# Optimization experiments

Hardware: AMD Instinct MI355X
Metric: run time of the kernel (lower is better)

The kernel has to match this reference:

```python
import jax, jax.numpy as jnp
import numpy as np

N = 50000        # num_node
P = 256          # nfeat
M = 128          # nhid
E = 800000       # num edges
KAPPA = 0.9
MITR = 20        # fixed-point iterations (orig: up to 300 w/ tol; fixed count for jit)
POWER_ITERS = 100


def proj_norm_inf(W, v):
    """Project each row of W onto the L1 ball of radius v (torch projection_norm_inf)."""
    m = W.shape[-1]
    a = jnp.abs(W)
    u = jnp.sort(a, axis=-1)[:, ::-1]                       # sorted desc
    cssv = jnp.cumsum(u, axis=-1) - v
    ind = jnp.arange(1, m + 1, dtype=W.dtype)
    rho = jnp.maximum(jnp.sum(u * ind > cssv, axis=-1), 1)
    theta = jnp.take_along_axis(cssv, (rho - 1)[:, None], axis=-1)[:, 0] / rho.astype(W.dtype)
    proj = jnp.sign(W) * jnp.maximum(a - theta[:, None], 0.0)
    return jnp.where((a.sum(-1) > v)[:, None], proj, W)


def spmm_AT(rows, cols, vals, Y):
    """A^T @ Y for COO A: out[c] = sum_e vals[e] * Y[rows[e]] where cols[e]==c. Y: [n, d]."""
    return jax.ops.segment_sum(vals[:, None] * Y[rows], cols, num_segments=N)


def spectral_rad(rows, cols, vals):
    """Power iteration for spectral radius of sparse A (torch get_spectral_rad)."""
    v0 = jnp.ones((N,), vals.dtype) / np.sqrt(N)

    def body(i, carry):
        v, _ = carry
        w = jax.ops.segment_sum(vals * v[cols], rows, num_segments=N)  # A @ v
        r = jnp.linalg.norm(w)
        return (w / (r + 1e-12), r)

    _, rho = jax.lax.fori_loop(0, POWER_ITERS, body, (v0, jnp.float32(1.0)))
    return jax.lax.stop_gradient(rho)


def implicit_graph(W, Omega, U, rows, cols, vals, adj_rho):
    """One ImplicitGraph layer: fixed point X = relu(W X A + Omega U A), X: [m, n]."""
    Wp = proj_norm_inf(W, KAPPA / adj_rho)
    # b_Omega = Omega @ U @ A, computed as (A^T @ (U^T @ Omega^T))^T : [m, n]
    B = spmm_AT(rows, cols, vals, U.T @ Omega.T).T

    def step(X, _):
        Xn = jax.nn.relu(spmm_AT(rows, cols, vals, (Wp @ X).T).T + B)
        return Xn, None

    X, _ = jax.lax.scan(jax.checkpoint(step), B, None, length=MITR)  # X_0 = b_Omega
    return X


def setup_inputs():
    key = jax.random.key(0)
    ks = jax.random.split(key, 10)
    s = lambda d: 1.0 / np.sqrt(d)
    return {
        "features": jax.random.normal(ks[0], (P, N), jnp.float32),
        "edge_vals": jax.random.uniform(ks[1], (E,), jnp.float32) * 0.1,
        "W1": jax.random.normal(ks[2], (M, M), jnp.float32) * s(M),
        "Omega1": jax.random.normal(ks[3], (M, P), jnp.float32) * s(P),
        "W2": jax.random.normal(ks[4], (M, M), jnp.float32) * s(M),
        "Omega2": jax.random.normal(ks[5], (M, M), jnp.float32) * s(M),
        "V0_w": jax.random.normal(ks[6], (M, P), jnp.float32) * s(P),
        "V0_b": jnp.zeros((M,), jnp.float32),
        "V1_w": jax.random.normal(ks[7], (M, M), jnp.float32) * s(M),
        "V1_b": jnp.zeros((M,), jnp.float32),
        "edge_rows": jax.random.randint(ks[8], (E,), 0, N),
        "edge_cols": jax.random.randint(ks[9], (E,), 0, N),
    }


def reference(features, edge_vals, W1, Omega1, W2, Omega2, V0_w, V0_b, V1_w, V1_b,
              edge_rows, edge_cols):
    adj_rho = spectral_rad(edge_rows, edge_cols, edge_vals)
    x = features                                                           # [p, n]
    h = implicit_graph(W1, Omega1, x, edge_rows, edge_cols, edge_vals, adj_rho)  # [m, n]
    x = jax.nn.elu(h.T + x.T @ V0_w.T + V0_b).T                            # [m, n]
    h = implicit_graph(W2, Omega2, x, edge_rows, edge_cols, edge_vals, adj_rho)
    out = h.T + x.T @ V1_w.T + V1_b                                        # [n, m]
    return out  # F.dropout is identity in eval mode
```

## Files before the change

### kernel.cpp

```cpp
#include <hip/hip_runtime.h>
#include <hip/hip_fp16.h>
#include <math.h>

#define NNODE 50000
#define NEDGE 800000
#define PITR  12
#define MITR  20
#define NBLK  196
#define NPAD  50048
#define ECAP  512

typedef _Float16 half8 __attribute__((ext_vector_type(8)));
typedef float floatx4 __attribute__((ext_vector_type(4)));


__global__ __launch_bounds__(256) void init_kernel(int* __restrict__ cnt_col,
                                                   float* __restrict__ wA,
                                                   float* __restrict__ norms) {
    int i = blockIdx.x * 256 + threadIdx.x;
    if (i < NNODE) { cnt_col[i] = 0; wA[i] = 1.0f; }
    if (i <= PITR) norms[i] = (i == 0) ? (float)NNODE : 0.0f;
}

__global__ __launch_bounds__(256) void count_kernel(const int* __restrict__ cols,
                                                    int* __restrict__ cnt_col) {
    int e = blockIdx.x * 256 + threadIdx.x;
    if (e < NEDGE) atomicAdd(&cnt_col[cols[e]], 1);
}

__global__ __launch_bounds__(256) void block_sums(const int* __restrict__ cnt,
                                                  int* __restrict__ bsum) {
    int i = blockIdx.x * 256 + threadIdx.x;
    int x = (i < NNODE) ? cnt[i] : 0;
    __shared__ int s[256];
    s[threadIdx.x] = x; __syncthreads();
    for (int off = 128; off; off >>= 1) {
        if (threadIdx.x < off) s[threadIdx.x] += s[threadIdx.x + off];
        __syncthreads();
    }
    if (threadIdx.x == 0) bsum[blockIdx.x] = s[0];
}

__global__ __launch_bounds__(256) void scan_partials(const int* __restrict__ bsum,
                                                     int* __restrict__ boff,
                                                     int* __restrict__ col_start) {
    __shared__ int s[256];
    int tid = threadIdx.x;
    int x = (tid < NBLK) ? bsum[tid] : 0;
    s[tid] = x; __syncthreads();
    for (int off = 1; off < 256; off <<= 1) {
        int t = (tid >= off) ? s[tid - off] : 0;
        __syncthreads();
        s[tid] += t;
        __syncthreads();
    }
    if (tid < NBLK) boff[tid] = s[tid] - x;
    if (tid == 255) col_start[NNODE] = s[255];
}

__global__ __launch_bounds__(256) void scan_final(const int* __restrict__ cnt,
                                                  const int* __restrict__ boff,
                                                  int* __restrict__ col_start,
                                                  int* __restrict__ cur) {
    int b = blockIdx.x, tid = threadIdx.x;
    int i = b * 256 + tid;
    int x = (i < NNODE) ? cnt[i] : 0;
    __shared__ int s[256];
    s[tid] = x; __syncthreads();
    for (int off = 1; off < 256; off <<= 1) {
        int t = (tid >= off) ? s[tid - off] : 0;
        __syncthreads();
        s[tid] += t;
        __syncthreads();
    }
    if (i < NNODE) { int excl = boff[b] + s[tid] - x; col_start[i] = excl; cur[i] = excl; }
}

__global__ __launch_bounds__(256) void fill_kernel(const int* __restrict__ rows,
                                                   const int* __restrict__ cols,
                                                   const float* __restrict__ vals,
                                                   int* __restrict__ cur_col,
                                                   int2* __restrict__ csc) {
    int e = blockIdx.x * 256 + threadIdx.x;
    if (e >= NEDGE) return;
    int c = cols[e];
    int pc = atomicAdd(&cur_col[c], 1);
    csc[pc] = make_int2(rows[e], __float_as_int(vals[e]));
}

__global__ __launch_bounds__(256) void spmv_pow(const int* __restrict__ col_start,
                                                const int2* __restrict__ csc,
                                                const float* __restrict__ wprev,
                                                float* __restrict__ wnew,
                                                const float* __restrict__ norm_in,
                                                float* __restrict__ norm_out) {
    int gid = blockIdx.x * 256 + threadIdx.x;
    int c = gid >> 2, sub = gid & 3;
    float inv = 1.0f / (sqrtf(*norm_in) + 1e-12f);
    float acc = 0.0f;
    if (c < NNODE) {
        int e0 = col_start[c], e1 = col_start[c + 1];
        for (int e = e0 + sub; e < e1; e += 4) {
            int2 ev = csc[e];
            acc += __int_as_float(ev.y) * wprev[ev.x];
        }
    }
    acc += __shfl_xor(acc, 1, 64);
    acc += __shfl_xor(acc, 2, 64);
    acc *= inv;
    float sq = (sub == 0 && c < NNODE) ? acc * acc : 0.0f;
    if (sub == 0 && c < NNODE) wnew[c] = acc;
    #pragma unroll
    for (int o = 32; o > 0; o >>= 1) sq += __shfl_down(sq, o, 64);
    __shared__ float wsum[4];
    int lane = threadIdx.x & 63, wv = threadIdx.x >> 6;
    if (lane == 0) wsum[wv] = sq;
    __syncthreads();
    if (threadIdx.x == 0) atomicAdd(norm_out, wsum[0] + wsum[1] + wsum[2] + wsum[3]);
}

__global__ __launch_bounds__(128) void proj_kernel(const float* __restrict__ Wa, const float* __restrict__ Wb,
                                                   __half* __restrict__ Oa, __half* __restrict__ Ob,
                                                   const float* __restrict__ norms) {
    __shared__ float u[128];
    __shared__ float sc[128];
    __shared__ float cs[128];
    __shared__ int ci[128];
    float rho = sqrtf(norms[PITR]);
    float vcap = 0.9f / rho;
    int which = blockIdx.x >> 7, row = blockIdx.x & 127;
    const float* W = which ? Wb : Wa;
    __half* O = which ? Ob : Oa;
    int j = threadIdx.x;
    float wv = W[row * 128 + j];
    float a = fabsf(wv);
    sc[j] = a; __syncthreads();
    for (int off = 64; off > 0; off >>= 1) {
        if (j < off) sc[j] += sc[j + off];
        __syncthreads();
    }
    float asum = sc[0];
    __syncthreads();
    if (asum <= vcap) { O[row * 128 + j] = (__half)wv; return; }
    u[j] = a; __syncthreads();
    for (int k = 2; k <= 128; k <<= 1) {
        for (int st = k >> 1; st > 0; st >>= 1) {
            int l = j ^ st;
            if (l > j) {
                float mine = u[j], other = u[l];
                bool sw = ((j & k) == 0) ? (mine < other) : (mine > other);
                if (sw) { u[j] = other; u[l] = mine; }
            }
            __syncthreads();
        }
    }
    sc[j] = u[j]; __syncthreads();
    for (int off = 1; off < 128; off <<= 1) {
        float t = (j >= off) ? sc[j - off] : 0.f;
        __syncthreads();
        sc[j] += t;
        __syncthreads();
    }
    float cssv = sc[j] - vcap;
    cs[j] = cssv;
    ci[j] = (u[j] * (float)(j + 1) > cssv) ? 1 : 0;
    __syncthreads();
    for (int off = 64; off > 0; off >>= 1) {
        if (j < off) ci[j] += ci[j + off];
        __syncthreads();
    }
    int cnt = ci[0]; if (cnt < 1) cnt = 1;
    float theta = cs[cnt - 1] / (float)cnt;
    float pr = fmaxf(a - theta, 0.f);
    O[row * 128 + j] = (__half)((wv < 0.f) ? -pr : pr);
}

__global__ __launch_bounds__(256) void wf_pack(const __half* __restrict__ Wp1, __half* __restrict__ Wf1,
                                               const __half* __restrict__ Wp2, __half* __restrict__ Wf2) {
    int which = blockIdx.x >> 3;
    int t = (blockIdx.x & 7) * 256 + threadIdx.x;
    const __half* Wp = which ? Wp2 : Wp1;
    __half* Wf = which ? Wf2 : Wf1;
    int lane = t & 63, frag = t >> 6;
    int ks = frag >> 3, it = frag & 7;
    int row = it * 16 + (lane & 15);
    int col = ks * 32 + (lane >> 4) * 8;
    *(uint4*)(Wf + (size_t)t * 8) = *(const uint4*)(Wp + (size_t)row * 128 + col);
}

template<int K>
__global__ __launch_bounds__(256) void wfpack32(const float* __restrict__ W, __half* __restrict__ Wf) {
    int t = blockIdx.x * 256 + threadIdx.x;
    int lane = t & 63, frag = t >> 6;
    int ks = frag >> 3, it = frag & 7;
    int row = it * 16 + (lane & 15);
    int col = ks * 32 + (lane >> 4) * 8;
    float4 a = *(const float4*)(W + (size_t)row * K + col);
    float4 b = *(const float4*)(W + (size_t)row * K + col + 4);
    union { uint4 u; __half2 h[4]; } pk;
    pk.h[0] = __float22half2_rn(make_float2(a.x, a.y));
    pk.h[1] = __float22half2_rn(make_float2(a.z, a.w));
    pk.h[2] = __float22half2_rn(make_float2(b.x, b.y));
    pk.h[3] = __float22half2_rn(make_float2(b.z, b.w));
    *(uint4*)(Wf + (size_t)t * 8) = pk.u;
}

__global__ __launch_bounds__(256) void feat_t(const float* __restrict__ F, __half* __restrict__ Fh, int n) {
    __shared__ unsigned short T[64 * 264];
    int nd0 = blockIdx.x * 64;
    int tid = threadIdx.x;
    for (int kk = 0; kk < 64; kk++) {
        int k = kk * 4 + (tid >> 6);
        int node = tid & 63;
        float v = (nd0 + node < n) ? F[(size_t)k * n + nd0 + node] : 0.f;
        __half h = (__half)v;
        T[node * 264 + k] = *(unsigned short*)&h;
    }
    __syncthreads();
    #pragma unroll
    for (int j = 0; j < 8; j++) {
        int row = j * 8 + (tid >> 5);
        int k8 = (tid & 31) * 8;
        uint4 v = *(const uint4*)&T[row * 264 + k8];
        if (nd0 + row < n) *(uint4*)(Fh + (size_t)(nd0 + row) * 256 + k8) = v;
    }
}

template<int K, int ACT, bool HASADD, bool HASBIAS, bool OUTF32>
__global__ __launch_bounds__(256) void gemmx(const _Float16* __restrict__ Wf,
                                             const _Float16* __restrict__ Xsrc,
                                             const __half* __restrict__ ADDh,
                                             const float* __restrict__ bias,
                                             void* __restrict__ Cout,
                                             int n) {
    __shared__ unsigned short Xs[128 * 136];
    int tid = threadIdx.x, wv = tid >> 6, lane = tid & 63;
    int node0 = blockIdx.x * 128;
    floatx4 acc[2][8];
    #pragma unroll
    for (int m = 0; m < 2; m++)
        #pragma unroll
        for (int it = 0; it < 8; it++) acc[m][it] = (floatx4)0.f;

    for (int kc = 0; kc < K; kc += 128) {
        if (kc) __syncthreads();
        #pragma unroll
        for (int j = 0; j < 8; j++) {
            int row = j * 16 + (tid >> 4), col = (tid & 15) * 8;
            uint4 v = *(const uint4*)(Xsrc + (size_t)(node0 + row) * K + kc + col);
            *(uint4*)&Xs[row * 136 + col] = v;
        }
        __syncthreads();
        int xrow = wv * 32 + (lane & 15), koff = (lane >> 4) * 8;
        #pragma unroll
        for (int ks = 0; ks < 4; ks++) {
            int k0 = ks * 32 + koff;
            half8 x0 = *(const half8*)&Xs[xrow * 136 + k0];
            half8 x1 = *(const half8*)&Xs[(xrow + 16) * 136 + k0];
            int ksg = (kc >> 5) + ks;
            #pragma unroll
            for (int it = 0; it < 8; it++) {
                half8 w = *(const half8*)(Wf + ((size_t)(ksg * 8 + it) * 64 + lane) * 8);
                acc[0][it] = __builtin_amdgcn_mfma_f32_16x16x32_f16(w, x0, acc[0][it], 0, 0, 0);
                acc[1][it] = __builtin_amdgcn_mfma_f32_16x16x32_f16(w, x1, acc[1][it], 0, 0, 0);
            }
        }
    }

    int i0 = (lane >> 4) * 4;
    #pragma unroll
    for (int m = 0; m < 2; m++) {
        int nl = wv * 32 + m * 16 + (lane & 15);
        int nd = node0 + nl;
        #pragma unroll
        for (int it = 0; it < 8; it++) {
            float o[4];
            #pragma unroll
            for (int r = 0; r < 4; r++) o[r] = acc[m][it][r];
            if (HASADD) {
                if (nd < n) {
                    union { uint2 u; __half2 h[2]; } av;
                    av.u = *(const uint2*)(ADDh + (size_t)nd * 128 + it * 16 + i0);
                    float2 a0 = __half22float2(av.h[0]), a1 = __half22float2(av.h[1]);
                    o[0] += a0.x; o[1] += a0.y; o[2] += a1.x; o[3] += a1.y;
                }
            }
            if (HASBIAS) {
                float4 bv = *(const float4*)(bias + it * 16 + i0);
                o[0] += bv.x; o[1] += bv.y; o[2] += bv.z; o[3] += bv.w;
            }
            if (ACT == 1) {
                #pragma unroll
                for (int r = 0; r < 4; r++) o[r] = fmaxf(o[r], 0.f);
            } else if (ACT == 2) {
                #pragma unroll
                for (int r = 0; r < 4; r++) o[r] = (o[r] > 0.f) ? o[r] : expm1f(o[r]);
            }
            union { uint2 u; __half2 h[2]; } pk;
            pk.h[0] = __float22half2_rn(make_float2(o[0], o[1]));
            pk.h[1] = __float22half2_rn(make_float2(o[2], o[3]));
            *(uint2*)&Xs[nl * 136 + it * 16 + i0] = pk.u;
        }
    }
    if (OUTF32) {
        float* C = (float*)Cout;
        #pragma unroll
        for (int j = 0; j < 16; j++) {
            int rl = wv * 32 + j * 2 + (lane >> 5);
            int nd2 = node0 + rl;
            int cb = (lane & 31) * 4;
            union { uint2 u; __half2 h[2]; } v;
            v.u = *(const uint2*)&Xs[rl * 136 + cb];
            float2 f0 = __half22float2(v.h[0]), f1 = __half22float2(v.h[1]);
            if (nd2 < n) *(float4*)(C + (size_t)nd2 * 128 + cb) = make_float4(f0.x, f0.y, f1.x, f1.y);
        }
    } else {
        __half* C = (__half*)Cout;
        #pragma unroll
        for (int j = 0; j < 8; j++) {
            int rl = wv * 32 + j * 4 + (lane >> 4);
            int nd2 = node0 + rl;
            uint4 v = *(const uint4*)&Xs[rl * 136 + (lane & 15) * 8];
            if (nd2 < n) *(uint4*)(C + (size_t)nd2 * 128 + (lane & 15) * 8) = v;
        }
    }
}

#define EPL 64
__global__ __launch_bounds__(256) void gather0(const int* __restrict__ col_start,
                                               const int2* __restrict__ csc,
                                               const __half* __restrict__ Zh,
                                               __half* __restrict__ Bh,
                                               __half* __restrict__ Xh,
                                               int n) {
    __shared__ int2 eds[4][EPL];
    int wv = threadIdx.x >> 6, lane = threadIdx.x & 63;
    int col = blockIdx.x * 4 + wv;
    int e0 = 0, e1 = 0;
    if (col < n) { e0 = col_start[col]; e1 = col_start[col + 1]; }
    int cnt = e1 - e0;
    int stage = cnt < EPL ? cnt : EPL;
    if (lane < stage) eds[wv][lane] = csc[e0 + lane];
    __syncthreads();
    if (col >= n) return;

    float2 acc = make_float2(0.f, 0.f);
    const uint* Zu = (const uint*)Zh;
    int j = 0;
    for (; j + 8 <= stage; j += 8) {
        int2 ev[8];
        #pragma unroll
        for (int q = 0; q < 8; q++) ev[q] = eds[wv][j + q];
        uint zb[8];
        #pragma unroll
        for (int q = 0; q < 8; q++) zb[q] = Zu[(size_t)ev[q].x * 64 + lane];
        #pragma unroll
        for (int q = 0; q < 8; q++) {
            float2 z = __half22float2(*(__half2*)&zb[q]);
            float v = __int_as_float(ev[q].y);
            acc.x += v * z.x;
            acc.y += v * z.y;
        }
    }
    for (; j < stage; j++) {
        int2 ev = eds[wv][j];
        uint zb = Zu[(size_t)ev.x * 64 + lane];
        float2 z = __half22float2(*(__half2*)&zb);
        float v = __int_as_float(ev.y);
        acc.x += v * z.x;
        acc.y += v * z.y;
    }
    for (int e = e0 + EPL; e < e1; e++) {
        int2 ev = csc[e];
        uint zb = Zu[(size_t)ev.x * 64 + lane];
        float2 z = __half22float2(*(__half2*)&zb);
        float v = __int_as_float(ev.y);
        acc.x += v * z.x;
        acc.y += v * z.y;
    }
    __half2 h = __float22half2_rn(acc);
    ((__half2*)Bh)[(size_t)col * 64 + lane] = h;
    ((__half2*)Xh)[(size_t)col * 64 + lane] = h;
}

__global__ __launch_bounds__(256) void iter_fused(const int* __restrict__ col_start,
                                                  const int2* __restrict__ csc,
                                                  const _Float16* __restrict__ Wf,
                                                  const __half* __restrict__ Xin,
                                                  const __half* __restrict__ Bh,
                                                  __half* __restrict__ Xout,
                                                  int n) {
    __shared__ unsigned short Gs[64 * 136];
    __shared__ int2 eds[4][ECAP];
    __shared__ int cst[4][17];
    int tid = threadIdx.x, wv = tid >> 6, lane = tid & 63;
    int node0 = blockIdx.x * 64;
    int c0 = node0 + wv * 16;
    const uint* Xu = (const uint*)Xin;

    if (lane < 17) {
        int idx = c0 + lane; if (idx > n) idx = n;
        cst[wv][lane] = col_start[idx];
    }
    int estart = cst[wv][0];
    int cnt = cst[wv][16] - estart;
    bool staged = (cnt <= ECAP);
    if (staged) {
        for (int i = lane; i < cnt; i += 64) eds[wv][i] = csc[estart + i];
    }

    for (int pp = 0; pp < 8; pp++) {
        int gA = cst[wv][2 * pp], gB = cst[wv][2 * pp + 1];
        int mA = gB - gA, mB = cst[wv][2 * pp + 2] - gB;
        int oA = gA - estart, oB = gB - estart;
        int lA = mA > 0 ? mA - 1 : 0, lB = mB > 0 ? mB - 1 : 0;
        int mx = mA > mB ? mA : mB;
        float2 aA = make_float2(0.f, 0.f), aB = make_float2(0.f, 0.f);
        if (staged) {
            for (int j = 0; j < mx; j += 8) {
                int2 evA[8], evB[8];
                #pragma unroll
                for (int q = 0; q < 8; q++) {
                    int ja = j + q; ja = ja < lA ? ja : lA;
                    int jb = j + q; jb = jb < lB ? jb : lB;
                    evA[q] = eds[wv][oA + ja];
                    evB[q] = eds[wv][oB + jb];
                }
                uint zA[8], zB[8];
                #pragma unroll
                for (int q = 0; q < 8; q++) zA[q] = Xu[(size_t)evA[q].x * 64 + lane];
                #pragma unroll
                for (int q = 0; q < 8; q++) zB[q] = Xu[(size_t)evB[q].x * 64 + lane];
                #pragma unroll
                for (int q = 0; q < 8; q++) {
                    float v = (j + q < mA) ? __int_as_float(evA[q].y) : 0.f;
                    float2 z = __half22float2(*(__half2*)&zA[q]);
                    aA.x += v * z.x; aA.y += v * z.y;
                }
                #pragma unroll
                for (int q = 0; q < 8; q++) {
                    float v = (j + q < mB) ? __int_as_float(evB[q].y) : 0.f;
                    float2 z = __half22float2(*(__half2*)&zB[q]);
                    aB.x += v * z.x; aB.y += v * z.y;
                }
            }
        } else {
            for (int j = 0; j < mx; j += 8) {
                int2 evA[8], evB[8];
                #pragma unroll
                for (int q = 0; q < 8; q++) {
                    int ja = j + q; ja = ja < lA ? ja : lA;
                    int jb = j + q; jb = jb < lB ? jb : lB;
                    evA[q] = csc[gA + ja];
                    evB[q] = csc[gB + jb];
                }
                uint zA[8], zB[8];
                #pragma unroll
                for (int q = 0; q < 8; q++) zA[q] = Xu[(size_t)evA[q].x * 64 + lane];
                #pragma unroll
                for (int q = 0; q < 8; q++) zB[q] = Xu[(size_t)evB[q].x * 64 + lane];
                #pragma unroll
                for (int q = 0; q < 8; q++) {
                    float v = (j + q < mA) ? __int_as_float(evA[q].y) : 0.f;
                    float2 z = __half22float2(*(__half2*)&zA[q]);
                    aA.x += v * z.x; aA.y += v * z.y;
                }
                #pragma unroll
                for (int q = 0; q < 8; q++) {
                    float v = (j + q < mB) ? __int_as_float(evB[q].y) : 0.f;
                    float2 z = __half22float2(*(__half2*)&zB[q]);
                    aB.x += v * z.x; aB.y += v * z.y;
                }
            }
        }
        *(__half2*)&Gs[(wv * 16 + pp * 2) * 136 + lane * 2] = __float22half2_rn(aA);
        *(__half2*)&Gs[(wv * 16 + pp * 2 + 1) * 136 + lane * 2] = __float22half2_rn(aB);
    }

    floatx4 acc[8];
    #pragma unroll
    for (int it = 0; it < 8; it++) acc[it] = (floatx4)0.f;
    int xrow = wv * 16 + (lane & 15);
    int koff = (lane >> 4) * 8;
    #pragma unroll
    for (int ks = 0; ks < 4; ks++) {
        int k0 = ks * 32 + koff;
        half8 g = *(const half8*)&Gs[xrow * 136 + k0];
        #pragma unroll
        for (int it = 0; it < 8; it++) {
            half8 w = *(const half8*)(Wf + ((size_t)(ks * 8 + it) * 64 + lane) * 8);
            acc[it] = __builtin_amdgcn_mfma_f32_16x16x32_f16(w, g, acc[it], 0, 0, 0);
        }
    }

    int nl = wv * 16 + (lane & 15);
    int i0 = (lane >> 4) * 4;
    int nd = node0 + nl;
    #pragma unroll
    for (int it = 0; it < 8; it++) {
        float o[4];
        #pragma unroll
        for (int r = 0; r < 4; r++) o[r] = acc[it][r];
        if (nd < n) {
            union { uint2 u; __half2 h[2]; } bv;
            bv.u = *(const uint2*)(Bh + (size_t)nd * 128 + it * 16 + i0);
            float2 b0 = __half22float2(bv.h[0]), b1 = __half22float2(bv.h[1]);
            o[0] += b0.x; o[1] += b0.y; o[2] += b1.x; o[3] += b1.y;
        }
        union { uint2 u; __half2 h[2]; } pk;
        pk.h[0] = __float22half2_rn(make_float2(fmaxf(o[0], 0.f), fmaxf(o[1], 0.f)));
        pk.h[1] = __float22half2_rn(make_float2(fmaxf(o[2], 0.f), fmaxf(o[3], 0.f)));
        *(uint2*)&Gs[nl * 136 + it * 16 + i0] = pk.u;
    }
    #pragma unroll
    for (int j = 0; j < 4; j++) {
        int rl = wv * 16 + j * 4 + (lane >> 4);
        int nd2 = node0 + rl;
        uint4 v = *(const uint4*)&Gs[rl * 136 + (lane & 15) * 8];
        if (nd2 < n) *(uint4*)(Xout + (size_t)nd2 * 128 + (lane & 15) * 8) = v;
    }
}


extern "C" void kernel_launch(void* const* d_in, const int* in_sizes, int n_in,
                              void* d_out, int out_size, void* d_ws, size_t ws_size,
                              hipStream_t stream) {
    (void)in_sizes; (void)n_in; (void)out_size; (void)ws_size;
    const float* features = (const float*)d_in[0];
    const float* edge_vals = (const float*)d_in[1];
    const float* W1 = (const float*)d_in[2];
    const float* Omega1 = (const float*)d_in[3];
    const float* W2 = (const float*)d_in[4];
    const float* Omega2 = (const float*)d_in[5];
    const float* V0w = (const float*)d_in[6];
    const float* V0b = (const float*)d_in[7];
    const float* V1w = (const float*)d_in[8];
    const float* V1b = (const float*)d_in[9];
    const int* erows = (const int*)d_in[10];
    const int* ecols = (const int*)d_in[11];
    float* out = (float*)d_out;
    const int n = NNODE;

    char* p = (char*)d_ws;
    auto alloc = [&](size_t bytes) -> void* {
        void* r = (void*)p;
        p += (bytes + 255) & ~(size_t)255;
        return r;
    };
    int* cnt_col = (int*)alloc(sizeof(int) * NNODE);
    int* col_start = (int*)alloc(sizeof(int) * (NNODE + 1));
    int* cur_col = (int*)alloc(sizeof(int) * NNODE);
    int* bsum = (int*)alloc(sizeof(int) * (NBLK + 1));
    int* boff = (int*)alloc(sizeof(int) * (NBLK + 1));
    int2* csc = (int2*)alloc(sizeof(int2) * NEDGE);
    float* wA = (float*)alloc(sizeof(float) * NNODE);
    float* wB = (float*)alloc(sizeof(float) * NNODE);
    float* norms = (float*)alloc(sizeof(float) * (PITR + 1));
    __half* Wp1h = (__half*)alloc(sizeof(__half) * 128 * 128);
    __half* Wp2h = (__half*)alloc(sizeof(__half) * 128 * 128);
    __half* Wf1 = (__half*)alloc(sizeof(__half) * 128 * 128);
    __half* Wf2 = (__half*)alloc(sizeof(__half) * 128 * 128);
    __half* WfO1 = (__half*)alloc(sizeof(__half) * 128 * 256);
    __half* WfV0 = (__half*)alloc(sizeof(__half) * 128 * 256);
    __half* WfO2 = (__half*)alloc(sizeof(__half) * 128 * 128);
    __half* WfV1 = (__half*)alloc(sizeof(__half) * 128 * 128);
    __half* Fh = (__half*)alloc(sizeof(__half) * (size_t)NPAD * 256);
    __half* Zh = (__half*)alloc(sizeof(__half) * (size_t)NPAD * 128);
    __half* Xa = (__half*)alloc(sizeof(__half) * (size_t)NPAD * 128);
    __half* Xb = (__half*)alloc(sizeof(__half) * (size_t)NPAD * 128);
    __half* Bh = (__half*)alloc(sizeof(__half) * (size_t)NPAD * 128);
    __half* x2h = (__half*)alloc(sizeof(__half) * (size_t)NPAD * 128);

    const int EB = (NEDGE + 255) / 256;
    const int NB = (NNODE + 255) / 256;
    init_kernel<<<NB, 256, 0, stream>>>(cnt_col, wA, norms);
    count_kernel<<<EB, 256, 0, stream>>>(ecols, cnt_col);
    block_sums<<<NBLK, 256, 0, stream>>>(cnt_col, bsum);
    scan_partials<<<1, 256, 0, stream>>>(bsum, boff, col_start);
    scan_final<<<NBLK, 256, 0, stream>>>(cnt_col, boff, col_start, cur_col);
    fill_kernel<<<EB, 256, 0, stream>>>(erows, ecols, edge_vals, cur_col, csc);
    const int PB = (NNODE * 4 + 255) / 256;
    for (int i = 0; i < PITR; i++) {
        float* wp = (i & 1) ? wB : wA;
        float* wn = (i & 1) ? wA : wB;
        spmv_pow<<<PB, 256, 0, stream>>>(col_start, csc, wp, wn, norms + i, norms + i + 1);
    }
    proj_kernel<<<256, 128, 0, stream>>>(W1, W2, Wp1h, Wp2h, norms);
    wf_pack<<<16, 256, 0, stream>>>(Wp1h, Wf1, Wp2h, Wf2);
    wfpack32<256><<<16, 256, 0, stream>>>(Omega1, WfO1);
    wfpack32<256><<<16, 256, 0, stream>>>(V0w, WfV0);
    wfpack32<128><<<8, 256, 0, stream>>>(Omega2, WfO2);
    wfpack32<128><<<8, 256, 0, stream>>>(V1w, WfV1);
    feat_t<<<(n + 63) / 64, 256, 0, stream>>>(features, Fh, n);

    const int GG = (n + 127) / 128;
    const int GI = (n + 63) / 64;
    const int GS = (n + 3) / 4;
    gemmx<256, 0, false, false, false><<<GG, 256, 0, stream>>>((const _Float16*)WfO1, (const _Float16*)Fh, nullptr, nullptr, Zh, n);
    gather0<<<GS, 256, 0, stream>>>(col_start, csc, Zh, Bh, Xa, n);
    for (int t = 0; t < MITR; t++) {
        const __half* src = (t & 1) ? Xb : Xa;
        __half* dst = (t & 1) ? Xa : Xb;
        iter_fused<<<GI, 256, 0, stream>>>(col_start, csc, (const _Float16*)Wf1, src, Bh, dst, n);
    }
    gemmx<256, 2, true, true, false><<<GG, 256, 0, stream>>>((const _Float16*)WfV0, (const _Float16*)Fh, Xa, V0b, x2h, n);
    gemmx<128, 0, false, false, false><<<GG, 256, 0, stream>>>((const _Float16*)WfO2, (const _Float16*)x2h, nullptr, nullptr, Zh, n);
    gather0<<<GS, 256, 0, stream>>>(col_start, csc, Zh, Bh, Xa, n);
    for (int t = 0; t < MITR; t++) {
        const __half* src = (t & 1) ? Xb : Xa;
        __half* dst = (t & 1) ? Xa : Xb;
        iter_fused<<<GI, 256, 0, stream>>>(col_start, csc, (const _Float16*)Wf2, src, Bh, dst, n);
    }
    gemmx<128, 0, true, true, true><<<GG, 256, 0, stream>>>((const _Float16*)WfV1, (const _Float16*)x2h, Xa, V1b, out, n);
}
```

Measured before the change: 2.204 ms.

## Shrink iter_fused blocks to 16 nodes with two cooperating waves

The fused SpMM+GEMM iteration kernel moves from 256-thread blocks, each wave independently handling 16 nodes, to 128-thread blocks covering 16 nodes. Both waves share the staged edge list and gather 8 nodes each, then each wave computes half of the 128 output channels in the MFMA step. The aim is to halve per-wave W fragment loads and accumulators, cut shared memory per block, and launch more, smaller blocks for better occupancy and load balance. In exchange it adds block-wide __syncthreads barriers and multiplies the number of blocks by four.

```diff
diff --git a/kernel.cpp b/kernel.cpp
--- a/kernel.cpp
+++ b/kernel.cpp
@@ -383,35 +383,37 @@
     ((__half2*)Xh)[(size_t)col * 64 + lane] = h;
 }
 
-__global__ __launch_bounds__(256) void iter_fused(const int* __restrict__ col_start,
+__global__ __launch_bounds__(128) void iter_fused(const int* __restrict__ col_start,
                                                   const int2* __restrict__ csc,
                                                   const _Float16* __restrict__ Wf,
                                                   const __half* __restrict__ Xin,
                                                   const __half* __restrict__ Bh,
                                                   __half* __restrict__ Xout,
                                                   int n) {
-    __shared__ unsigned short Gs[64 * 136];
-    __shared__ int2 eds[4][ECAP];
-    __shared__ int cst[4][17];
+    __shared__ unsigned short Gs[16 * 136];
+    __shared__ int2 eds[ECAP];
+    __shared__ int cst[17];
     int tid = threadIdx.x, wv = tid >> 6, lane = tid & 63;
-    int node0 = blockIdx.x * 64;
-    int c0 = node0 + wv * 16;
+    int node0 = blockIdx.x * 16;
     const uint* Xu = (const uint*)Xin;
 
-    if (lane < 17) {
-        int idx = c0 + lane; if (idx > n) idx = n;
-        cst[wv][lane] = col_start[idx];
-    }
-    int estart = cst[wv][0];
-    int cnt = cst[wv][16] - estart;
+    if (tid < 17) {
+        int idx = node0 + tid; if (idx > n) idx = n;
+        cst[tid] = col_start[idx];
+    }
+    __syncthreads();
+    int estart = cst[0];
+    int cnt = cst[16] - estart;
     bool staged = (cnt <= ECAP);
     if (staged) {
-        for (int i = lane; i < cnt; i += 64) eds[wv][i] = csc[estart + i];
-    }
-
-    for (int pp = 0; pp < 8; pp++) {
-        int gA = cst[wv][2 * pp], gB = cst[wv][2 * pp + 1];
-        int mA = gB - gA, mB = cst[wv][2 * pp + 2] - gB;
+        for (int i = tid; i < cnt; i += 128) eds[i] = csc[estart + i];
+    }
+    __syncthreads();
+
+    for (int pp = 0; pp < 4; pp++) {
+        int ca = wv * 8 + pp * 2;
+        int gA = cst[ca], gB = cst[ca + 1], gC = cst[ca + 2];
+        int mA = gB - gA, mB = gC - gB;
         int oA = gA - estart, oB = gB - estart;
         int lA = mA > 0 ? mA - 1 : 0, lB = mB > 0 ? mB - 1 : 0;
         int mx = mA > mB ? mA : mB;
@@ -423,8 +425,8 @@
                 for (int q = 0; q < 8; q++) {
                     int ja = j + q; ja = ja < lA ? ja : lA;
                     int jb = j + q; jb = jb < lB ? jb : lB;
-                    evA[q] = eds[wv][oA + ja];
-                    evB[q] = eds[wv][oB + jb];
+                    evA[q] = eds[oA + ja];
+                    evB[q] = eds[oB + jb];
                 }
                 uint zA[8], zB[8];
                 #pragma unroll
@@ -473,34 +475,37 @@
                 }
             }
         }
-        *(__half2*)&Gs[(wv * 16 + pp * 2) * 136 + lane * 2] = __float22half2_rn(aA);
-        *(__half2*)&Gs[(wv * 16 + pp * 2 + 1) * 136 + lane * 2] = __float22half2_rn(aB);
-    }
-
-    floatx4 acc[8];
-    #pragma unroll
-    for (int it = 0; it < 8; it++) acc[it] = (floatx4)0.f;
-    int xrow = wv * 16 + (lane & 15);
+        *(__half2*)&Gs[ca * 136 + lane * 2] = __float22half2_rn(aA);
+        *(__half2*)&Gs[(ca + 1) * 136 + lane * 2] = __float22half2_rn(aB);
+    }
+    __syncthreads();
+
+    floatx4 acc[4];
+    #pragma unroll
+    for (int itl = 0; itl < 4; itl++) acc[itl] = (floatx4)0.f;
+    int xrow = lane & 15;
     int koff = (lane >> 4) * 8;
     #pragma unroll
     for (int ks = 0; ks < 4; ks++) {
         int k0 = ks * 32 + koff;
         half8 g = *(const half8*)&Gs[xrow * 136 + k0];
         #pragma unroll
-        for (int it = 0; it < 8; it++) {
+        for (int itl = 0; itl < 4; itl++) {
+            int it = wv * 4 + itl;
             half8 w = *(const half8*)(Wf + ((size_t)(ks * 8 + it) * 64 + lane) * 8);
-            acc[it] = __builtin_amdgcn_mfma_f32_16x16x32_f16(w, g, acc[it], 0, 0, 0);
-        }
-    }
-
-    int nl = wv * 16 + (lane & 15);
+            acc[itl] = __builtin_amdgcn_mfma_f32_16x16x32_f16(w, g, acc[itl], 0, 0, 0);
+        }
+    }
+
+    int nl = lane & 15;
     int i0 = (lane >> 4) * 4;
     int nd = node0 + nl;
     #pragma unroll
-    for (int it = 0; it < 8; it++) {
+    for (int itl = 0; itl < 4; itl++) {
+        int it = wv * 4 + itl;
         float o[4];
         #pragma unroll
-        for (int r = 0; r < 4; r++) o[r] = acc[it][r];
+        for (int r = 0; r < 4; r++) o[r] = acc[itl][r];
         if (nd < n) {
             union { uint2 u; __half2 h[2]; } bv;
             bv.u = *(const uint2*)(Bh + (size_t)nd * 128 + it * 16 + i0);
@@ -512,12 +517,14 @@
         pk.h[1] = __float22half2_rn(make_float2(fmaxf(o[2], 0.f), fmaxf(o[3], 0.f)));
         *(uint2*)&Gs[nl * 136 + it * 16 + i0] = pk.u;
     }
-    #pragma unroll
-    for (int j = 0; j < 4; j++) {
-        int rl = wv * 16 + j * 4 + (lane >> 4);
-        int nd2 = node0 + rl;
-        uint4 v = *(const uint4*)&Gs[rl * 136 + (lane & 15) * 8];
-        if (nd2 < n) *(uint4*)(Xout + (size_t)nd2 * 128 + (lane & 15) * 8) = v;
+    __syncthreads();
+    #pragma unroll
+    for (int j = 0; j < 2; j++) {
+        int u = j * 128 + tid;
+        int row = u >> 4, seg = u & 15;
+        int nd2 = node0 + row;
+        uint4 v = *(const uint4*)&Gs[row * 136 + seg * 8];
+        if (nd2 < n) *(uint4*)(Xout + (size_t)nd2 * 128 + seg * 8) = v;
     }
 }
 
@@ -594,14 +601,14 @@
     feat_t<<<(n + 63) / 64, 256, 0, stream>>>(features, Fh, n);
 
     const int GG = (n + 127) / 128;
-    const int GI = (n + 63) / 64;
+    const int GI = (n + 15) / 16;
     const int GS = (n + 3) / 4;
     gemmx<256, 0, false, false, false><<<GG, 256, 0, stream>>>((const _Float16*)WfO1, (const _Float16*)Fh, nullptr, nullptr, Zh, n);
     gather0<<<GS, 256, 0, stream>>>(col_start, csc, Zh, Bh, Xa, n);
     for (int t = 0; t < MITR; t++) {
         const __half* src = (t & 1) ? Xb : Xa;
         __half* dst = (t & 1) ? Xa : Xb;
-        iter_fused<<<GI, 256, 0, stream>>>(col_start, csc, (const _Float16*)Wf1, src, Bh, dst, n);
+        iter_fused<<<GI, 128, 0, stream>>>(col_start, csc, (const _Float16*)Wf1, src, Bh, dst, n);
     }
     gemmx<256, 2, true, true, false><<<GG, 256, 0, stream>>>((const _Float16*)WfV0, (const _Float16*)Fh, Xa, V0b, x2h, n);
     gemmx<128, 0, false, false, false><<<GG, 256, 0, stream>>>((const _Float16*)WfO2, (const _Float16*)x2h, nullptr, nullptr, Zh, n);
@@ -609,7 +616,7 @@
     for (int t = 0; t < MITR; t++) {
         const __half* src = (t & 1) ? Xb : Xa;
         __half* dst = (t & 1) ? Xa : Xb;
-        iter_fused<<<GI, 256, 0, stream>>>(col_start, csc, (const _Float16*)Wf2, src, Bh, dst, n);
+        iter_fused<<<GI, 128, 0, stream>>>(col_start, csc, (const _Float16*)Wf2, src, Bh, dst, n);
     }
     gemmx<128, 0, true, true, true><<<GG, 256, 0, stream>>>((const _Float16*)WfV1, (const _Float16*)x2h, Xa, V1b, out, n);
 }
```

Result: faster. 1.951 ms (-11.5%).
